# Kernel optimization log

Hardware: AMD Instinct MI355X
Metric: run time of the kernel (lower is better)

## Reference

```python
import jax, jax.numpy as jnp
import numpy as np

B, H, W, C = 16, 128, 128, 256
C8 = C // 8


def setup_inputs() -> dict:
    key = jax.random.key(0)
    ks = jax.random.split(key, 7)
    s = 0.02
    return {
        "x": jax.random.normal(ks[0], (B, H, W, C), dtype=jnp.float32),
        "wq": jax.random.normal(ks[1], (C, C8), dtype=jnp.float32) * s,
        "bq": jnp.zeros((C8,), dtype=jnp.float32),
        "wk": jax.random.normal(ks[2], (C, C8), dtype=jnp.float32) * s,
        "bk": jnp.zeros((C8,), dtype=jnp.float32),
        "wv": jax.random.normal(ks[3], (C, C), dtype=jnp.float32) * s,
        "bv": jnp.zeros((C,), dtype=jnp.float32),
    }


def reference(x, wq, bq, wk, bk, wv, bv):
    # 1x1 convs == per-pixel linear projections
    q = jnp.einsum("bhwc,cd->bhwd", x, wq) + bq  # [B,H,W,C/8]
    k = jnp.einsum("bhwc,cd->bhwd", x, wk) + bk  # [B,H,W,C/8]
    v = jnp.einsum("bhwc,cd->bhwd", x, wv) + bv  # [B,H,W,C]
    # tf.matmul on 4D: batch over (B,H), attention over W (row-wise)
    scores = jnp.einsum("bhwd,bhvd->bhwv", q, k)  # [B,H,W,W]
    attn = jax.nn.softmax(scores, axis=-1)
    out = jnp.einsum("bhwv,bhvc->bhwc", attn, v)  # [B,H,W,C]
    return out
```

## Files before the change

### kernel.cpp

```cpp
#include <hip/hip_runtime.h>

typedef __attribute__((ext_vector_type(8))) short short8;
typedef __attribute__((ext_vector_type(16))) float f32x16;
typedef __attribute__((ext_vector_type(4))) float float4v;
typedef __attribute__((ext_vector_type(4))) unsigned u32x4;
typedef __attribute__((ext_vector_type(4))) unsigned short ushort4v;
typedef unsigned short u16;

#define MFMA32(a, b, c) __builtin_amdgcn_mfma_f32_32x32x16_bf16((a), (b), (c), 0, 0, 0)

#define W_ 128
#define C_ 256
#define X_LD 136
#define VT_LD 136
#define QK_LD 40

__device__ __forceinline__ u16 f2bf(float f) {
    unsigned u = __builtin_bit_cast(unsigned, f);
    u += 0x7fffu + ((u >> 16) & 1u);
    return (u16)(u >> 16);
}

__device__ __forceinline__ f32x16 zero16() {
    f32x16 z;
#pragma unroll
    for (int i = 0; i < 16; ++i) z[i] = 0.f;
    return z;
}

__device__ __forceinline__ void gll16(const u16* g, const u16* l) {
    auto s = (const __attribute__((address_space(1))) unsigned*)((uintptr_t)g);
    auto d = (__attribute__((address_space(3))) unsigned*)((unsigned)(uintptr_t)l);
    __builtin_amdgcn_global_load_lds(s, d, 16, 0, 0);
}

__device__ __forceinline__ void wg_barrier() {
    asm volatile("s_waitcnt lgkmcnt(0)" ::: "memory");
    __builtin_amdgcn_sched_barrier(0);
    __builtin_amdgcn_s_barrier();
    __builtin_amdgcn_sched_barrier(0);
}

__global__ __launch_bounds__(256) void prep_pack(const float* __restrict__ wq,
                                                 const float* __restrict__ wk,
                                                 const float* __restrict__ wv,
                                                 u16* __restrict__ pack) {
    int t = blockIdx.x * 256 + threadIdx.x;
    int j = t & 7;
    int l = (t >> 3) & 63;
    int g = t >> 9;
    int f = g % 10;
    int ks = g / 10;
    int k = ks * 16 + ((l >> 5) << 3) + j;
    int c = l & 31;
    float w;
    if (f == 0)      w = wq[k * 32 + c];
    else if (f == 1) w = wk[k * 32 + c];
    else             w = wv[k * 256 + (f - 2) * 32 + c];
    pack[t] = f2bf(w);
}

__global__ __launch_bounds__(256, 2) void attn_fused(
        const float* __restrict__ x,
        const u16* __restrict__ pack,
        const float* __restrict__ bq, const float* __restrict__ bk,
        const float* __restrict__ bv,
        float* __restrict__ out) {
    __shared__ u16 uA[17408];
    __shared__ u16 uC[17408];

    const int slice = blockIdx.x;
    const int tid = threadIdx.x;
    const int lane = tid & 63;
    const int wid = tid >> 6;
    const int lm = lane & 31;
    const int l5 = lane >> 5;
    const int rowbase = wid * 32;
    const float* xs = x + (size_t)slice * (W_ * C_);

    const u16* vw0 = pack + (size_t)(2 + wid) * 512 + lane * 8;
    const u16* vw1 = pack + (size_t)(2 + wid + 4) * 512 + lane * 8;

    f32x16 qa = zero16();
    f32x16 ka = zero16();
    f32x16 vac0[4], vac1[4];
#pragma unroll
    for (int nn = 0; nn < 4; ++nn) { vac0[nn] = zero16(); vac1[nn] = zero16(); }

#pragma unroll
    for (int i = 0; i < 4; ++i) {
        int ks = wid * 4 + i;
        const u16* gs = pack + (size_t)ks * 5120 + lane * 8;
        gll16(gs, &uC[(ks * 2 + 0) * 512]);
        gll16(gs + 512, &uC[(ks * 2 + 1) * 512]);
    }

    for (int c = 0; c < 2; ++c) {
        if (c == 1) wg_barrier();
        {
            int r0 = tid >> 5;
            int col = (tid & 31) * 4;
#pragma unroll
            for (int p = 0; p < 16; ++p) {
                int row = p * 8 + r0;
                float4v xv = *reinterpret_cast<const float4v*>(xs + row * C_ + c * 128 + col);
                ushort4v b4;
                b4[0] = f2bf(xv[0]); b4[1] = f2bf(xv[1]);
                b4[2] = f2bf(xv[2]); b4[3] = f2bf(xv[3]);
                *reinterpret_cast<ushort4v*>(&uA[row * X_LD + col]) = b4;
            }
        }
        __syncthreads();

        short8 wf0[4], wf1[4];
        wf0[0] = *reinterpret_cast<const short8*>(vw0 + (size_t)(c * 8 + 0) * 5120);
        wf1[0] = *reinterpret_cast<const short8*>(vw1 + (size_t)(c * 8 + 0) * 5120);
        wf0[1] = *reinterpret_cast<const short8*>(vw0 + (size_t)(c * 8 + 1) * 5120);
        wf1[1] = *reinterpret_cast<const short8*>(vw1 + (size_t)(c * 8 + 1) * 5120);

#pragma unroll
        for (int kt = 0; kt < 8; ++kt) {
            const int ks = c * 8 + kt;
            if (kt < 6) {
                wf0[(kt + 2) & 3] = *reinterpret_cast<const short8*>(vw0 + (size_t)(ks + 2) * 5120);
                wf1[(kt + 2) & 3] = *reinterpret_cast<const short8*>(vw1 + (size_t)(ks + 2) * 5120);
            }
            short8 xf[4];
#pragma unroll
            for (int nn = 0; nn < 4; ++nn)
                xf[nn] = *reinterpret_cast<const short8*>(&uA[(nn * 32 + lm) * X_LD + kt * 16 + l5 * 8]);
            short8 aqk = *reinterpret_cast<const short8*>(&uA[(rowbase + lm) * X_LD + kt * 16 + l5 * 8]);
            short8 bq8 = *reinterpret_cast<const short8*>(&uC[(ks * 2 + 0) * 512 + lane * 8]);
            short8 bk8 = *reinterpret_cast<const short8*>(&uC[(ks * 2 + 1) * 512 + lane * 8]);
            qa = MFMA32(aqk, bq8, qa);
            ka = MFMA32(aqk, bk8, ka);
#pragma unroll
            for (int nn = 0; nn < 4; ++nn) {
                vac0[nn] = MFMA32(wf0[kt & 3], xf[nn], vac0[nn]);
                vac1[nn] = MFMA32(wf1[kt & 3], xf[nn], vac1[nn]);
            }
        }
    }
    wg_barrier();

    {
        float bqv = bq[lm];
        float bkv = bk[lm];
#pragma unroll
        for (int e = 0; e < 16; ++e) {
            int row = rowbase + (e & 3) + 8 * (e >> 2) + 4 * l5;
            uC[row * QK_LD + lm] = f2bf(qa[e] + bqv);
            uC[5120 + row * QK_LD + lm] = f2bf(ka[e] + bkv);
        }
    }
#pragma unroll
    for (int e = 0; e < 16; ++e) {
        int cl = (e & 3) + 8 * (e >> 2) + 4 * l5;
        float bvv = bv[wid * 32 + cl];
#pragma unroll
        for (int nn = 0; nn < 4; ++nn)
            uA[(wid * 32 + cl) * VT_LD + nn * 32 + lm] = f2bf(vac0[nn][e] + bvv);
    }
    wg_barrier();

    f32x16 sT[4];
#pragma unroll
    for (int c2 = 0; c2 < 4; ++c2) sT[c2] = zero16();
#pragma unroll
    for (int ktd = 0; ktd < 2; ++ktd) {
        short8 qf = *reinterpret_cast<const short8*>(&uC[(rowbase + lm) * QK_LD + ktd * 16 + l5 * 8]);
#pragma unroll
        for (int c2 = 0; c2 < 4; ++c2) {
            short8 kf = *reinterpret_cast<const short8*>(&uC[5120 + (c2 * 32 + lm) * QK_LD + ktd * 16 + l5 * 8]);
            sT[c2] = MFMA32(kf, qf, sT[c2]);
        }
    }

    float m = sT[0][0];
#pragma unroll
    for (int c2 = 0; c2 < 4; ++c2)
#pragma unroll
        for (int e = 0; e < 16; ++e) m = fmaxf(m, sT[c2][e]);
    m = fmaxf(m, __shfl_xor(m, 32));
    float sum = 0.f;
#pragma unroll
    for (int c2 = 0; c2 < 4; ++c2)
#pragma unroll
        for (int e = 0; e < 16; ++e) {
            float v = __expf(sT[c2][e] - m);
            sT[c2][e] = v;
            sum += v;
        }
    sum += __shfl_xor(sum, 32);
    const float inv = 1.0f / sum;

    short8 pf[8];
#pragma unroll
    for (int c2 = 0; c2 < 4; ++c2) {
        unsigned bpk[8];
#pragma unroll
        for (int i = 0; i < 8; ++i)
            bpk[i] = (unsigned)f2bf(sT[c2][2 * i] * inv) |
                     ((unsigned)f2bf(sT[c2][2 * i + 1] * inv) << 16);
#pragma unroll
        for (int hh = 0; hh < 2; ++hh) {
            unsigned s0 = l5 ? bpk[4 * hh + 0] : bpk[4 * hh + 2];
            unsigned s1 = l5 ? bpk[4 * hh + 1] : bpk[4 * hh + 3];
            unsigned t0 = (unsigned)__shfl_xor((int)s0, 32);
            unsigned t1 = (unsigned)__shfl_xor((int)s1, 32);
            union { u32x4 u; short8 s; } fr;
            fr.u[0] = l5 ? t0 : bpk[4 * hh + 0];
            fr.u[1] = l5 ? t1 : bpk[4 * hh + 1];
            fr.u[2] = l5 ? bpk[4 * hh + 2] : t0;
            fr.u[3] = l5 ? bpk[4 * hh + 3] : t1;
            pf[2 * c2 + hh] = fr.s;
        }
    }

    float* os = out + (size_t)slice * (W_ * C_);

    f32x16 oc[4];
#pragma unroll
    for (int c2 = 0; c2 < 4; ++c2) oc[c2] = zero16();
#pragma unroll
    for (int kt16 = 0; kt16 < 8; ++kt16) {
#pragma unroll
        for (int c2 = 0; c2 < 4; ++c2) {
            short8 vb = *reinterpret_cast<const short8*>(&uA[(c2 * 32 + lm) * VT_LD + kt16 * 16 + l5 * 8]);
            oc[c2] = MFMA32(pf[kt16], vb, oc[c2]);
        }
    }
    wg_barrier();

#pragma unroll
    for (int e = 0; e < 16; ++e) {
        int cl = (e & 3) + 8 * (e >> 2) + 4 * l5;
        float bvv = bv[128 + wid * 32 + cl];
#pragma unroll
        for (int nn = 0; nn < 4; ++nn)
            uA[(wid * 32 + cl) * VT_LD + nn * 32 + lm] = f2bf(vac1[nn][e] + bvv);
    }
#pragma unroll
    for (int c2 = 0; c2 < 4; ++c2)
#pragma unroll
        for (int e = 0; e < 16; ++e) {
            int row = rowbase + (e & 3) + 8 * (e >> 2) + 4 * l5;
            os[row * C_ + c2 * 32 + lm] = oc[c2][e];
        }
    wg_barrier();

#pragma unroll
    for (int c2 = 0; c2 < 4; ++c2) oc[c2] = zero16();
#pragma unroll
    for (int kt16 = 0; kt16 < 8; ++kt16) {
#pragma unroll
        for (int c2 = 0; c2 < 4; ++c2) {
            short8 vb = *reinterpret_cast<const short8*>(&uA[(c2 * 32 + lm) * VT_LD + kt16 * 16 + l5 * 8]);
            oc[c2] = MFMA32(pf[kt16], vb, oc[c2]);
        }
    }
#pragma unroll
    for (int c2 = 0; c2 < 4; ++c2)
#pragma unroll
        for (int e = 0; e < 16; ++e) {
            int row = rowbase + (e & 3) + 8 * (e >> 2) + 4 * l5;
            os[row * C_ + 128 + c2 * 32 + lm] = oc[c2][e];
        }
}

extern "C" void kernel_launch(void* const* d_in, const int* in_sizes, int n_in,
                              void* d_out, int out_size, void* d_ws, size_t ws_size,
                              hipStream_t stream) {
    const float* x  = (const float*)d_in[0];
    const float* wq = (const float*)d_in[1];
    const float* bq = (const float*)d_in[2];
    const float* wk = (const float*)d_in[3];
    const float* bk = (const float*)d_in[4];
    const float* wv = (const float*)d_in[5];
    const float* bv = (const float*)d_in[6];
    float* out = (float*)d_out;
    u16* pack = (u16*)d_ws;

    prep_pack<<<320, 256, 0, stream>>>(wq, wk, wv, pack);
    attn_fused<<<2048, 256, 0, stream>>>(x, pack, bq, bk, bv, out);
}
```

Before: 148.4 us.

## Software-pipeline x loads in 64-channel chunks with register prefetch

Splits the projection's K loop into four 64-channel chunks. The next chunk of x is prefetched from global memory into registers while MFMAs run on the current chunk in LDS, which hides global load latency. The x tile stride shrinks and uC is trimmed, so LDS use drops. It adds a barrier per chunk and raises register pressure from the eight float4 prefetch registers. It also moves the first half's output stores before the V-transpose write so they can overlap.

```diff
diff --git a/kernel.cpp b/kernel.cpp
--- a/kernel.cpp
+++ b/kernel.cpp
@@ -11,7 +11,7 @@
 
 #define W_ 128
 #define C_ 256
-#define X_LD 136
+#define X_LD 72
 #define VT_LD 136
 #define QK_LD 40
 
@@ -67,7 +67,7 @@
         const float* __restrict__ bv,
         float* __restrict__ out) {
     __shared__ u16 uA[17408];
-    __shared__ u16 uC[17408];
+    __shared__ u16 uC[16384];
 
     const int slice = blockIdx.x;
     const int tid = threadIdx.x;
@@ -81,12 +81,19 @@
     const u16* vw0 = pack + (size_t)(2 + wid) * 512 + lane * 8;
     const u16* vw1 = pack + (size_t)(2 + wid + 4) * 512 + lane * 8;
 
+    const int r0x = tid >> 4;
+    const int colx = (tid & 15) * 4;
+
     f32x16 qa = zero16();
     f32x16 ka = zero16();
     f32x16 vac0[4], vac1[4];
 #pragma unroll
     for (int nn = 0; nn < 4; ++nn) { vac0[nn] = zero16(); vac1[nn] = zero16(); }
 
+    float4v xv[8];
+#pragma unroll
+    for (int p = 0; p < 8; ++p)
+        xv[p] = *reinterpret_cast<const float4v*>(xs + (p * 16 + r0x) * C_ + colx);
 #pragma unroll
     for (int i = 0; i < 4; ++i) {
         int ks = wid * 4 + i;
@@ -94,36 +101,38 @@
         gll16(gs, &uC[(ks * 2 + 0) * 512]);
         gll16(gs + 512, &uC[(ks * 2 + 1) * 512]);
     }
-
-    for (int c = 0; c < 2; ++c) {
-        if (c == 1) wg_barrier();
-        {
-            int r0 = tid >> 5;
-            int col = (tid & 31) * 4;
-#pragma unroll
-            for (int p = 0; p < 16; ++p) {
-                int row = p * 8 + r0;
-                float4v xv = *reinterpret_cast<const float4v*>(xs + row * C_ + c * 128 + col);
-                ushort4v b4;
-                b4[0] = f2bf(xv[0]); b4[1] = f2bf(xv[1]);
-                b4[2] = f2bf(xv[2]); b4[3] = f2bf(xv[3]);
-                *reinterpret_cast<ushort4v*>(&uA[row * X_LD + col]) = b4;
-            }
-        }
-        __syncthreads();
-
-        short8 wf0[4], wf1[4];
-        wf0[0] = *reinterpret_cast<const short8*>(vw0 + (size_t)(c * 8 + 0) * 5120);
-        wf1[0] = *reinterpret_cast<const short8*>(vw1 + (size_t)(c * 8 + 0) * 5120);
-        wf0[1] = *reinterpret_cast<const short8*>(vw0 + (size_t)(c * 8 + 1) * 5120);
-        wf1[1] = *reinterpret_cast<const short8*>(vw1 + (size_t)(c * 8 + 1) * 5120);
-
-#pragma unroll
-        for (int kt = 0; kt < 8; ++kt) {
-            const int ks = c * 8 + kt;
-            if (kt < 6) {
-                wf0[(kt + 2) & 3] = *reinterpret_cast<const short8*>(vw0 + (size_t)(ks + 2) * 5120);
-                wf1[(kt + 2) & 3] = *reinterpret_cast<const short8*>(vw1 + (size_t)(ks + 2) * 5120);
+#pragma unroll
+    for (int p = 0; p < 8; ++p) {
+        int row = p * 16 + r0x;
+        ushort4v b4;
+        b4[0] = f2bf(xv[p][0]); b4[1] = f2bf(xv[p][1]);
+        b4[2] = f2bf(xv[p][2]); b4[3] = f2bf(xv[p][3]);
+        *reinterpret_cast<ushort4v*>(&uA[row * X_LD + colx]) = b4;
+    }
+    __syncthreads();
+
+    short8 wf0[4], wf1[4];
+    wf0[0] = *reinterpret_cast<const short8*>(vw0 + (size_t)0 * 5120);
+    wf1[0] = *reinterpret_cast<const short8*>(vw1 + (size_t)0 * 5120);
+    wf0[1] = *reinterpret_cast<const short8*>(vw0 + (size_t)1 * 5120);
+    wf1[1] = *reinterpret_cast<const short8*>(vw1 + (size_t)1 * 5120);
+
+#pragma unroll
+    for (int c = 0; c < 4; ++c) {
+        if (c < 3) {
+#pragma unroll
+            for (int p = 0; p < 8; ++p)
+                xv[p] = *reinterpret_cast<const float4v*>(
+                    xs + (p * 16 + r0x) * C_ + (c + 1) * 64 + colx);
+        }
+        __builtin_amdgcn_sched_barrier(0);
+
+#pragma unroll
+        for (int kt = 0; kt < 4; ++kt) {
+            const int ks = c * 4 + kt;
+            if (ks < 14) {
+                wf0[(ks + 2) & 3] = *reinterpret_cast<const short8*>(vw0 + (size_t)(ks + 2) * 5120);
+                wf1[(ks + 2) & 3] = *reinterpret_cast<const short8*>(vw1 + (size_t)(ks + 2) * 5120);
             }
             short8 xf[4];
 #pragma unroll
@@ -136,9 +145,22 @@
             ka = MFMA32(aqk, bk8, ka);
 #pragma unroll
             for (int nn = 0; nn < 4; ++nn) {
-                vac0[nn] = MFMA32(wf0[kt & 3], xf[nn], vac0[nn]);
-                vac1[nn] = MFMA32(wf1[kt & 3], xf[nn], vac1[nn]);
+                vac0[nn] = MFMA32(wf0[ks & 3], xf[nn], vac0[nn]);
+                vac1[nn] = MFMA32(wf1[ks & 3], xf[nn], vac1[nn]);
             }
+        }
+
+        if (c < 3) {
+            wg_barrier();
+#pragma unroll
+            for (int p = 0; p < 8; ++p) {
+                int row = p * 16 + r0x;
+                ushort4v b4;
+                b4[0] = f2bf(xv[p][0]); b4[1] = f2bf(xv[p][1]);
+                b4[2] = f2bf(xv[p][2]); b4[3] = f2bf(xv[p][3]);
+                *reinterpret_cast<ushort4v*>(&uA[row * X_LD + colx]) = b4;
+            }
+            __syncthreads();
         }
     }
     wg_barrier();
@@ -233,6 +255,13 @@
     wg_barrier();
 
 #pragma unroll
+    for (int c2 = 0; c2 < 4; ++c2)
+#pragma unroll
+        for (int e = 0; e < 16; ++e) {
+            int row = rowbase + (e & 3) + 8 * (e >> 2) + 4 * l5;
+            os[row * C_ + c2 * 32 + lm] = oc[c2][e];
+        }
+#pragma unroll
     for (int e = 0; e < 16; ++e) {
         int cl = (e & 3) + 8 * (e >> 2) + 4 * l5;
         float bvv = bv[128 + wid * 32 + cl];
@@ -240,13 +269,6 @@
         for (int nn = 0; nn < 4; ++nn)
             uA[(wid * 32 + cl) * VT_LD + nn * 32 + lm] = f2bf(vac1[nn][e] + bvv);
     }
-#pragma unroll
-    for (int c2 = 0; c2 < 4; ++c2)
-#pragma unroll
-        for (int e = 0; e < 16; ++e) {
-            int row = rowbase + (e & 3) + 8 * (e >> 2) + 4 * l5;
-            os[row * C_ + c2 * 32 + lm] = oc[c2][e];
-        }
     wg_barrier();
 
 #pragma unroll
```

Result: faster. 133.5 us (-10.0%).
